# Kernel tuning notes

Measured on AMD Instinct MI355X. Metric: run time of the kernel, lower is better.

The kernel has to match this reference:

```python
import jax, jax.numpy as jnp
import numpy as np

EPS = 1e-7  # utils.add_dummy(eps=True) dummy value


def setup_inputs() -> dict:
    key = jax.random.key(0)
    ks = jax.random.split(key, 8)
    n_mentions, emb = 8192, 1024
    batch, n_ants, pw_emb = 1024, 50, 64
    pair_emb = 3 * emb + pw_emb  # 3136
    hidden = 1024
    return {
        "all_mentions": jax.random.normal(ks[0], (n_mentions, emb), jnp.float32),
        "mentions_batch": jax.random.normal(ks[1], (batch, emb), jnp.float32),
        "pw_batch": jax.random.normal(ks[2], (batch, n_ants, pw_emb), jnp.float32),
        "top_rough_scores_batch": jax.random.normal(ks[3], (batch, n_ants), jnp.float32),
        "W1": jax.random.normal(ks[4], (pair_emb, hidden), jnp.float32) * 0.02,
        "b1": jnp.zeros((hidden,), jnp.float32),
        "W_out": jax.random.normal(ks[5], (hidden, 1), jnp.float32) * 0.02,
        "b_out": jnp.zeros((1,), jnp.float32),
        "top_indices_batch": jax.random.randint(ks[6], (batch, n_ants), 0, n_mentions, jnp.int64),
    }


def reference(all_mentions, mentions_batch, pw_batch, top_rough_scores_batch,
              W1, b1, W_out, b_out, top_indices_batch):
    # gather antecedent embeddings: [batch, n_ants, emb]
    b_mentions = all_mentions[top_indices_batch]
    a_mentions = jnp.broadcast_to(mentions_batch[:, None, :], b_mentions.shape)
    # pair matrix: [batch, n_ants, 3*emb + pw_emb]
    pair = jnp.concatenate([a_mentions, b_mentions, a_mentions * b_mentions, pw_batch], axis=2)
    # FFNN: Linear -> LeakyReLU (dropout is identity in eval) -> Linear(->1)
    h = jax.nn.leaky_relu(jnp.einsum("bnf,fh->bnh", pair, W1) + b1, negative_slope=0.01)
    ffnn = (jnp.einsum("bnh,ho->bno", h, W_out) + b_out)[..., 0]  # [batch, n_ants]
    scores = top_rough_scores_batch + ffnn
    dummy = jnp.full((scores.shape[0], 1), EPS, scores.dtype)
    return jnp.concatenate([dummy, scores], axis=1)  # [batch, n_ants + 1]
```

## Files before the change

### kernel.cpp

```cpp
#include <hip/hip_runtime.h>
#include <cstdint>


typedef short short8 __attribute__((ext_vector_type(8)));
typedef float f32x4 __attribute__((ext_vector_type(4)));

#define BT_STRIDE 100352
#define MT_STRIDE 32768
#define PT_STRIDE 34816

static __device__ __forceinline__ unsigned short f2bf(float x) {
  union { float f; unsigned u; } v; v.f = x;
  unsigned r = v.u + 0x7fffu + ((v.u >> 16) & 1u);
  return (unsigned short)(r >> 16);
}
static __device__ __forceinline__ float bf2f(unsigned short u) {
  union { unsigned u; float f; } v; v.u = ((unsigned)u) << 16;
  return v.f;
}

__global__ void k_packW(const float* __restrict__ W1, unsigned short* __restrict__ BtAll) {
  __shared__ float t[64][65];
  int k0 = blockIdx.x * 64, n0 = blockIdx.y * 64;
  int c = threadIdx.x & 63, r4 = threadIdx.x >> 6;
#pragma unroll
  for (int rr = 0; rr < 16; ++rr) {
    int r = rr * 4 + r4;
    t[r][c] = W1[(size_t)(k0 + r) * 1024 + n0 + c];
  }
  __syncthreads();
#pragma unroll
  for (int qq = 0; qq < 2; ++qq) {
    int q = threadIdx.x * 2 + qq;
    int cc = q >> 3, rg = q & 7;
    short8 v;
#pragma unroll
    for (int e = 0; e < 8; ++e) v[e] = (short)f2bf(t[rg * 8 + e][cc]);
    int ct = (n0 + cc) >> 4;
    int kc = (k0 >> 5) + (rg >> 2);
    int ln = (cc & 15) + ((rg & 3) << 4);
    *(short8*)((char*)BtAll + (size_t)ct * BT_STRIDE + kc * 1024 + ln * 16) = v;
  }
}

__global__ void k_cvt(const float* __restrict__ s, unsigned short* __restrict__ d, int n4) {
  int i = blockIdx.x * 256 + threadIdx.x;
  if (i < n4) {
    float4 v = ((const float4*)s)[i];
    ushort4 o; o.x = f2bf(v.x); o.y = f2bf(v.y); o.z = f2bf(v.z); o.w = f2bf(v.w);
    ((ushort4*)d)[i] = o;
  }
}

__global__ void k_packM(const float* __restrict__ am, const float* __restrict__ allm,
                        unsigned short* __restrict__ Mt) {
  int rt = blockIdx.x, t = threadIdx.x;
  const float* S = (rt < 512) ? (allm + (size_t)rt * 16 * 1024)
                              : (am + (size_t)(rt - 512) * 16 * 1024);
  int pf = t & 15, oct = (t >> 4) & 3, kcl = t >> 6;
  const float* row = S + (size_t)pf * 1024;
  char* dst = (char*)Mt + (size_t)rt * MT_STRIDE + (t & 63) * 16;
#pragma unroll
  for (int pass = 0; pass < 8; ++pass) {
    int kc = pass * 4 + kcl;
    int k = kc * 32 + oct * 8;
    float4 v0 = *(const float4*)(row + k);
    float4 v1 = *(const float4*)(row + k + 4);
    short8 o;
    o[0] = (short)f2bf(v0.x); o[1] = (short)f2bf(v0.y);
    o[2] = (short)f2bf(v0.z); o[3] = (short)f2bf(v0.w);
    o[4] = (short)f2bf(v1.x); o[5] = (short)f2bf(v1.y);
    o[6] = (short)f2bf(v1.z); o[7] = (short)f2bf(v1.w);
    *(short8*)(dst + kc * 1024) = o;
  }
}

__global__ void k_pairs(const unsigned short* __restrict__ Abm,
                        const unsigned short* __restrict__ Aball,
                        const float* __restrict__ pw, const int* __restrict__ idx,
                        unsigned short* __restrict__ Pt) {
  __shared__ int g16[16];
  int rt = blockIdx.x, t = threadIdx.x;
  if (t < 16) g16[t] = idx[rt * 16 + t];
  __syncthreads();
  int pf = t & 15, oct = (t >> 4) & 3, kcl = t >> 6;
  int p = rt * 16 + pf;
  const unsigned short* arow = Abm + (size_t)(p / 50) * 1024;
  const unsigned short* brow = Aball + (size_t)g16[pf] * 1024;
  char* dst = (char*)Pt + (size_t)rt * PT_STRIDE + (t & 63) * 16;
#pragma unroll
  for (int pass = 0; pass < 8; ++pass) {
    int kc = pass * 4 + kcl;
    int k = kc * 32 + oct * 8;
    short8 a8 = *(const short8*)(arow + k);
    short8 b8 = *(const short8*)(brow + k);
    short8 o;
#pragma unroll
    for (int e = 0; e < 8; ++e)
      o[e] = (short)f2bf(bf2f((unsigned short)a8[e]) * bf2f((unsigned short)b8[e]));
    *(short8*)(dst + kc * 1024) = o;
  }
  if (t < 128) {
    int kc = 32 + (t >> 6);
    int kpw = (t >> 6) * 32 + oct * 8;
    const float* prow = pw + (size_t)p * 64;
    float4 v0 = *(const float4*)(prow + kpw);
    float4 v1 = *(const float4*)(prow + kpw + 4);
    short8 o;
    o[0] = (short)f2bf(v0.x); o[1] = (short)f2bf(v0.y);
    o[2] = (short)f2bf(v0.z); o[3] = (short)f2bf(v0.w);
    o[4] = (short)f2bf(v1.x); o[5] = (short)f2bf(v1.y);
    o[6] = (short)f2bf(v1.z); o[7] = (short)f2bf(v1.w);
    *(short8*)(dst + kc * 1024) = o;
  }
}

template <int MODE>
__global__ __launch_bounds__(256, 2) void k_gt(
    const unsigned short* __restrict__ At, const unsigned short* __restrict__ BtAll,
    float* __restrict__ C, float* __restrict__ partial,
    const float* __restrict__ Hab, const float* __restrict__ b1,
    const float* __restrict__ Wout, const int* __restrict__ idx) {
  constexpr int NKC = MODE ? 34 : 32;
  constexpr int A_STRIDE = MODE ? PT_STRIDE : MT_STRIDE;
  int tid = threadIdx.x, lane = tid & 63, wave = tid >> 6;
  int llo = lane & 15, lhi = lane >> 4;
  int id = blockIdx.x;
  int x, y;
  if (MODE == 1) {
    int r = id >> 3;
    x = (id & 7) * 100 + (r >> 1);
    y = r & 1;
  } else {
    x = id >> 1;
    y = id & 1;
  }
  int kcoff = MODE ? 64 : ((x < 128) ? 32 : 0);
  int row0 = x * 64;
  int n0w = y * 512 + wave * 128;
  const char* pa = (const char*)At + (size_t)(row0 >> 4) * A_STRIDE + lane * 16;
  const char* pb = (const char*)BtAll + (size_t)(n0w >> 4) * BT_STRIDE +
                   (size_t)kcoff * 1024 + lane * 16;

  f32x4 acc[4][8] = {};
  short8 aA[4], bA[8], aB[4], bB[8];
#pragma unroll
  for (int m = 0; m < 4; ++m) aA[m] = *(const short8*)(pa + (size_t)m * A_STRIDE);
#pragma unroll
  for (int n = 0; n < 8; ++n) bA[n] = *(const short8*)(pb + (size_t)n * BT_STRIDE);
  for (int kt = 0; kt < NKC; kt += 2) {
#pragma unroll
    for (int m = 0; m < 4; ++m)
      aB[m] = *(const short8*)(pa + (size_t)m * A_STRIDE + (kt + 1) * 1024);
#pragma unroll
    for (int n = 0; n < 8; ++n)
      bB[n] = *(const short8*)(pb + (size_t)n * BT_STRIDE + (kt + 1) * 1024);
#pragma unroll
    for (int m = 0; m < 4; ++m)
#pragma unroll
      for (int n = 0; n < 8; ++n)
        acc[m][n] = __builtin_amdgcn_mfma_f32_16x16x32_bf16(aA[m], bA[n], acc[m][n], 0, 0, 0);
    if (kt + 2 < NKC) {
#pragma unroll
      for (int m = 0; m < 4; ++m)
        aA[m] = *(const short8*)(pa + (size_t)m * A_STRIDE + (kt + 2) * 1024);
#pragma unroll
      for (int n = 0; n < 8; ++n)
        bA[n] = *(const short8*)(pb + (size_t)n * BT_STRIDE + (kt + 2) * 1024);
    }
#pragma unroll
    for (int m = 0; m < 4; ++m)
#pragma unroll
      for (int n = 0; n < 8; ++n)
        acc[m][n] = __builtin_amdgcn_mfma_f32_16x16x32_bf16(aB[m], bB[n], acc[m][n], 0, 0, 0);
  }

  if (MODE == 0) {
#pragma unroll
    for (int m = 0; m < 4; ++m)
#pragma unroll
      for (int i = 0; i < 4; ++i) {
        int row = row0 + m * 16 + lhi * 4 + i;
#pragma unroll
        for (int n = 0; n < 8; ++n)
          C[(size_t)row * 1024 + n0w + n * 16 + llo] = acc[m][n][i];
      }
  } else {
    float b1v[8], wov[8];
    int coln[8];
#pragma unroll
    for (int n = 0; n < 8; ++n) {
      coln[n] = n0w + n * 16 + llo;
      b1v[n] = b1[coln[n]];
      wov[n] = Wout[coln[n]];
    }
    int chunk = n0w >> 6;
#pragma unroll
    for (int m = 0; m < 4; ++m)
#pragma unroll
      for (int i = 0; i < 4; ++i) {
        int p = row0 + m * 16 + lhi * 4 + i;
        int bb = p / 50;
        int gg = idx[p];
        const float* Har = Hab + (size_t)(8192 + bb) * 1024;
        const float* Hbr = Hab + (size_t)gg * 1024;
        float s0 = 0.f, s1 = 0.f;
#pragma unroll
        for (int n = 0; n < 4; ++n) {
          float h = acc[m][n][i] + Har[coln[n]] + Hbr[coln[n]] + b1v[n];
          h = h > 0.f ? h : 0.01f * h;
          s0 += h * wov[n];
        }
#pragma unroll
        for (int n = 4; n < 8; ++n) {
          float h = acc[m][n][i] + Har[coln[n]] + Hbr[coln[n]] + b1v[n];
          h = h > 0.f ? h : 0.01f * h;
          s1 += h * wov[n];
        }
        s0 += __shfl_xor(s0, 1, 64);
        s0 += __shfl_xor(s0, 2, 64);
        s0 += __shfl_xor(s0, 4, 64);
        s0 += __shfl_xor(s0, 8, 64);
        s1 += __shfl_xor(s1, 1, 64);
        s1 += __shfl_xor(s1, 2, 64);
        s1 += __shfl_xor(s1, 4, 64);
        s1 += __shfl_xor(s1, 8, 64);
        if (llo == 0) {
          partial[(size_t)p * 16 + chunk + 0] = s0;
          partial[(size_t)p * 16 + chunk + 1] = s1;
        }
      }
  }
}

__global__ void k_final(const float* __restrict__ partial, const float* __restrict__ rough,
                        const float* __restrict__ bout, float* __restrict__ out) {
  int t = blockIdx.x * 256 + threadIdx.x;
  if (t < 51200) {
    float s = rough[t] + bout[0];
    const float* pp = partial + (size_t)t * 16;
#pragma unroll
    for (int c = 0; c < 16; ++c) s += pp[c];
    out[(size_t)(t / 50) * 51 + 1 + (t % 50)] = s;
  }
  if (t < 1024) out[(size_t)t * 51] = 1e-7f;
}

extern "C" void kernel_launch(void* const* d_in, const int* in_sizes, int n_in,
                              void* d_out, int out_size, void* d_ws, size_t ws_size,
                              hipStream_t stream) {
  (void)in_sizes; (void)n_in; (void)out_size;
  const float* allm  = (const float*)d_in[0];
  const float* am    = (const float*)d_in[1];
  const float* pw    = (const float*)d_in[2];
  const float* rough = (const float*)d_in[3];
  const float* W1    = (const float*)d_in[4];
  const float* b1    = (const float*)d_in[5];
  const float* Wout  = (const float*)d_in[6];
  const float* bout  = (const float*)d_in[7];
  const int*   idx   = (const int*)d_in[8];
  float* out = (float*)d_out;

  char* w = (char*)d_ws;
  unsigned short* BtAll = (unsigned short*)w; w += (size_t)64 * BT_STRIDE;
  unsigned short* Mt    = (unsigned short*)w; w += (size_t)576 * MT_STRIDE;
  unsigned short* Abm   = (unsigned short*)w; w += (size_t)1024 * 1024 * 2;
  unsigned short* Aball = (unsigned short*)w; w += (size_t)8192 * 1024 * 2;
  unsigned short* Pt    = (unsigned short*)w; w += (size_t)3200 * PT_STRIDE;
  float* Hab            = (float*)w;          w += (size_t)9216 * 1024 * 4;
  float* part           = (float*)w;          w += (size_t)51200 * 16 * 4;
  size_t need = (size_t)(w - (char*)d_ws);
  if (ws_size < need) return;

  k_packW<<<dim3(49, 16), 256, 0, stream>>>(W1, BtAll);
  k_cvt<<<dim3(1024), 256, 0, stream>>>(am, Abm, 1024 * 1024 / 4);
  k_cvt<<<dim3(8192), 256, 0, stream>>>(allm, Aball, 8192 * 1024 / 4);
  k_packM<<<dim3(576), 256, 0, stream>>>(am, allm, Mt);
  k_pairs<<<dim3(3200), 256, 0, stream>>>(Abm, Aball, pw, idx, Pt);
  k_gt<0><<<dim3(288), 256, 0, stream>>>(Mt, BtAll, Hab, nullptr,
                                         nullptr, nullptr, nullptr, nullptr);
  k_gt<1><<<dim3(1600), 256, 0, stream>>>(Pt, BtAll, nullptr, part,
                                          Hab, b1, Wout, idx);
  k_final<<<dim3(200), 256, 0, stream>>>(part, rough, bout, out);
}
```

Before: 254.1 us.

## Enlarge GEMM wave tiles to 128x128 with interleaved fragment layout

```diff
diff --git a/kernel.cpp b/kernel.cpp
--- a/kernel.cpp
+++ b/kernel.cpp
@@ -5,9 +5,9 @@
 typedef short short8 __attribute__((ext_vector_type(8)));
 typedef float f32x4 __attribute__((ext_vector_type(4)));
 
-#define BT_STRIDE 100352
-#define MT_STRIDE 32768
-#define PT_STRIDE 34816
+#define PT2_RT 278528ULL
+#define MT2_RT 262144ULL
+#define BT2_CT 802816ULL
 
 static __device__ __forceinline__ unsigned short f2bf(float x) {
   union { float f; unsigned u; } v; v.f = x;
@@ -19,7 +19,7 @@
   return v.f;
 }
 
-__global__ void k_packW(const float* __restrict__ W1, unsigned short* __restrict__ BtAll) {
+__global__ void k_packW(const float* __restrict__ W1, unsigned short* __restrict__ Bt2) {
   __shared__ float t[64][65];
   int k0 = blockIdx.x * 64, n0 = blockIdx.y * 64;
   int c = threadIdx.x & 63, r4 = threadIdx.x >> 6;
@@ -36,10 +36,11 @@
     short8 v;
 #pragma unroll
     for (int e = 0; e < 8; ++e) v[e] = (short)f2bf(t[rg * 8 + e][cc]);
-    int ct = (n0 + cc) >> 4;
+    int col = n0 + cc;
+    int ct = col >> 7, nf = (col >> 4) & 7;
     int kc = (k0 >> 5) + (rg >> 2);
-    int ln = (cc & 15) + ((rg & 3) << 4);
-    *(short8*)((char*)BtAll + (size_t)ct * BT_STRIDE + kc * 1024 + ln * 16) = v;
+    int ln = (col & 15) + ((rg & 3) << 4);
+    *(short8*)((char*)Bt2 + (size_t)ct * BT2_CT + (size_t)kc * 8192 + nf * 1024 + ln * 16) = v;
   }
 }
 
@@ -53,13 +54,14 @@
 }
 
 __global__ void k_packM(const float* __restrict__ am, const float* __restrict__ allm,
-                        unsigned short* __restrict__ Mt) {
-  int rt = blockIdx.x, t = threadIdx.x;
-  const float* S = (rt < 512) ? (allm + (size_t)rt * 16 * 1024)
-                              : (am + (size_t)(rt - 512) * 16 * 1024);
+                        unsigned short* __restrict__ Mt2) {
+  int bid = blockIdx.x, t = threadIdx.x;
+  int rt = bid >> 3, mf = bid & 7;
   int pf = t & 15, oct = (t >> 4) & 3, kcl = t >> 6;
-  const float* row = S + (size_t)pf * 1024;
-  char* dst = (char*)Mt + (size_t)rt * MT_STRIDE + (t & 63) * 16;
+  int grow = bid * 16 + pf;
+  const float* row = (grow < 8192) ? (allm + (size_t)grow * 1024)
+                                   : (am + (size_t)(grow - 8192) * 1024);
+  char* dst = (char*)Mt2 + (size_t)rt * MT2_RT + mf * 1024 + (t & 63) * 16;
 #pragma unroll
   for (int pass = 0; pass < 8; ++pass) {
     int kc = pass * 4 + kcl;
@@ -71,23 +73,25 @@
     o[2] = (short)f2bf(v0.z); o[3] = (short)f2bf(v0.w);
     o[4] = (short)f2bf(v1.x); o[5] = (short)f2bf(v1.y);
     o[6] = (short)f2bf(v1.z); o[7] = (short)f2bf(v1.w);
-    *(short8*)(dst + kc * 1024) = o;
+    *(short8*)(dst + (size_t)kc * 8192) = o;
   }
 }
 
 __global__ void k_pairs(const unsigned short* __restrict__ Abm,
                         const unsigned short* __restrict__ Aball,
                         const float* __restrict__ pw, const int* __restrict__ idx,
-                        unsigned short* __restrict__ Pt) {
+                        unsigned short* __restrict__ Pt2) {
   __shared__ int g16[16];
-  int rt = blockIdx.x, t = threadIdx.x;
-  if (t < 16) g16[t] = idx[rt * 16 + t];
+  int bid = blockIdx.x, t = threadIdx.x;
+  int rt = bid >> 3, mf = bid & 7;
+  int p0 = bid * 16;
+  if (t < 16) g16[t] = idx[p0 + t];
   __syncthreads();
   int pf = t & 15, oct = (t >> 4) & 3, kcl = t >> 6;
-  int p = rt * 16 + pf;
+  int p = p0 + pf;
   const unsigned short* arow = Abm + (size_t)(p / 50) * 1024;
   const unsigned short* brow = Aball + (size_t)g16[pf] * 1024;
-  char* dst = (char*)Pt + (size_t)rt * PT_STRIDE + (t & 63) * 16;
+  char* dst = (char*)Pt2 + (size_t)rt * PT2_RT + mf * 1024 + (t & 63) * 16;
 #pragma unroll
   for (int pass = 0; pass < 8; ++pass) {
     int kc = pass * 4 + kcl;
@@ -98,7 +102,7 @@
 #pragma unroll
     for (int e = 0; e < 8; ++e)
       o[e] = (short)f2bf(bf2f((unsigned short)a8[e]) * bf2f((unsigned short)b8[e]));
-    *(short8*)(dst + kc * 1024) = o;
+    *(short8*)(dst + (size_t)kc * 8192) = o;
   }
   if (t < 128) {
     int kc = 32 + (t >> 6);
@@ -111,65 +115,69 @@
     o[2] = (short)f2bf(v0.z); o[3] = (short)f2bf(v0.w);
     o[4] = (short)f2bf(v1.x); o[5] = (short)f2bf(v1.y);
     o[6] = (short)f2bf(v1.z); o[7] = (short)f2bf(v1.w);
-    *(short8*)(dst + kc * 1024) = o;
+    *(short8*)(dst + (size_t)kc * 8192) = o;
   }
 }
 
 template <int MODE>
-__global__ __launch_bounds__(256, 2) void k_gt(
-    const unsigned short* __restrict__ At, const unsigned short* __restrict__ BtAll,
+__global__ __launch_bounds__(256, 1) void k_gt(
+    const unsigned short* __restrict__ At, const unsigned short* __restrict__ Bt2,
     float* __restrict__ C, float* __restrict__ partial,
     const float* __restrict__ Hab, const float* __restrict__ b1,
     const float* __restrict__ Wout, const int* __restrict__ idx) {
   constexpr int NKC = MODE ? 34 : 32;
-  constexpr int A_STRIDE = MODE ? PT_STRIDE : MT_STRIDE;
+  constexpr size_t ART = MODE ? PT2_RT : MT2_RT;
   int tid = threadIdx.x, lane = tid & 63, wave = tid >> 6;
+  int wr = wave >> 1, wc = wave & 1;
   int llo = lane & 15, lhi = lane >> 4;
   int id = blockIdx.x;
   int x, y;
   if (MODE == 1) {
     int r = id >> 3;
-    x = (id & 7) * 100 + (r >> 1);
-    y = r & 1;
+    x = (id & 7) * 25 + (r >> 2);
+    y = r & 3;
   } else {
-    x = id >> 1;
-    y = id & 1;
-  }
-  int kcoff = MODE ? 64 : ((x < 128) ? 32 : 0);
-  int row0 = x * 64;
-  int n0w = y * 512 + wave * 128;
-  const char* pa = (const char*)At + (size_t)(row0 >> 4) * A_STRIDE + lane * 16;
-  const char* pb = (const char*)BtAll + (size_t)(n0w >> 4) * BT_STRIDE +
-                   (size_t)kcoff * 1024 + lane * 16;
-
-  f32x4 acc[4][8] = {};
-  short8 aA[4], bA[8], aB[4], bB[8];
-#pragma unroll
-  for (int m = 0; m < 4; ++m) aA[m] = *(const short8*)(pa + (size_t)m * A_STRIDE);
-#pragma unroll
-  for (int n = 0; n < 8; ++n) bA[n] = *(const short8*)(pb + (size_t)n * BT_STRIDE);
+    x = id >> 2;
+    y = id & 3;
+  }
+  int kcoff = MODE ? 64 : ((x < 32) ? 32 : 0);
+  int rt = x * 2 + wr;
+  int ct = y * 2 + wc;
+  int row0 = rt * 128;
+  int n0w = ct * 128;
+  const char* pa = (const char*)At + (size_t)rt * ART + lane * 16;
+  const char* pb = (const char*)Bt2 + (size_t)ct * BT2_CT + (size_t)kcoff * 8192 + lane * 16;
+
+  f32x4 acc[8][8] = {};
+  short8 aA[8], bA[8], aB[8], bB[8];
+#pragma unroll
+  for (int m = 0; m < 8; ++m) aA[m] = *(const short8*)(pa + m * 1024);
+#pragma unroll
+  for (int n = 0; n < 8; ++n) bA[n] = *(const short8*)(pb + n * 1024);
   for (int kt = 0; kt < NKC; kt += 2) {
-#pragma unroll
-    for (int m = 0; m < 4; ++m)
-      aB[m] = *(const short8*)(pa + (size_t)m * A_STRIDE + (kt + 1) * 1024);
-#pragma unroll
-    for (int n = 0; n < 8; ++n)
-      bB[n] = *(const short8*)(pb + (size_t)n * BT_STRIDE + (kt + 1) * 1024);
-#pragma unroll
-    for (int m = 0; m < 4; ++m)
+    {
+      const char* pa1 = pa + (size_t)(kt + 1) * 8192;
+      const char* pb1 = pb + (size_t)(kt + 1) * 8192;
+#pragma unroll
+      for (int m = 0; m < 8; ++m) aB[m] = *(const short8*)(pa1 + m * 1024);
+#pragma unroll
+      for (int n = 0; n < 8; ++n) bB[n] = *(const short8*)(pb1 + n * 1024);
+    }
+#pragma unroll
+    for (int m = 0; m < 8; ++m)
 #pragma unroll
       for (int n = 0; n < 8; ++n)
         acc[m][n] = __builtin_amdgcn_mfma_f32_16x16x32_bf16(aA[m], bA[n], acc[m][n], 0, 0, 0);
     if (kt + 2 < NKC) {
-#pragma unroll
-      for (int m = 0; m < 4; ++m)
-        aA[m] = *(const short8*)(pa + (size_t)m * A_STRIDE + (kt + 2) * 1024);
-#pragma unroll
-      for (int n = 0; n < 8; ++n)
-        bA[n] = *(const short8*)(pb + (size_t)n * BT_STRIDE + (kt + 2) * 1024);
+      const char* pa2 = pa + (size_t)(kt + 2) * 8192;
+      const char* pb2 = pb + (size_t)(kt + 2) * 8192;
+#pragma unroll
+      for (int m = 0; m < 8; ++m) aA[m] = *(const short8*)(pa2 + m * 1024);
+#pragma unroll
+      for (int n = 0; n < 8; ++n) bA[n] = *(const short8*)(pb2 + n * 1024);
     }
 #pragma unroll
-    for (int m = 0; m < 4; ++m)
+    for (int m = 0; m < 8; ++m)
 #pragma unroll
       for (int n = 0; n < 8; ++n)
         acc[m][n] = __builtin_amdgcn_mfma_f32_16x16x32_bf16(aB[m], bB[n], acc[m][n], 0, 0, 0);
@@ -177,7 +185,7 @@
 
   if (MODE == 0) {
 #pragma unroll
-    for (int m = 0; m < 4; ++m)
+    for (int m = 0; m < 8; ++m)
 #pragma unroll
       for (int i = 0; i < 4; ++i) {
         int row = row0 + m * 16 + lhi * 4 + i;
@@ -196,7 +204,7 @@
     }
     int chunk = n0w >> 6;
 #pragma unroll
-    for (int m = 0; m < 4; ++m)
+    for (int m = 0; m < 8; ++m)
 #pragma unroll
       for (int i = 0; i < 4; ++i) {
         int p = row0 + m * 16 + lhi * 4 + i;
@@ -262,24 +270,24 @@
   float* out = (float*)d_out;
 
   char* w = (char*)d_ws;
-  unsigned short* BtAll = (unsigned short*)w; w += (size_t)64 * BT_STRIDE;
-  unsigned short* Mt    = (unsigned short*)w; w += (size_t)576 * MT_STRIDE;
+  unsigned short* Bt2   = (unsigned short*)w; w += (size_t)8 * BT2_CT;
+  unsigned short* Mt2   = (unsigned short*)w; w += (size_t)72 * MT2_RT;
   unsigned short* Abm   = (unsigned short*)w; w += (size_t)1024 * 1024 * 2;
   unsigned short* Aball = (unsigned short*)w; w += (size_t)8192 * 1024 * 2;
-  unsigned short* Pt    = (unsigned short*)w; w += (size_t)3200 * PT_STRIDE;
+  unsigned short* Pt2   = (unsigned short*)w; w += (size_t)400 * PT2_RT;
   float* Hab            = (float*)w;          w += (size_t)9216 * 1024 * 4;
   float* part           = (float*)w;          w += (size_t)51200 * 16 * 4;
   size_t need = (size_t)(w - (char*)d_ws);
   if (ws_size < need) return;
 
-  k_packW<<<dim3(49, 16), 256, 0, stream>>>(W1, BtAll);
+  k_packW<<<dim3(49, 16), 256, 0, stream>>>(W1, Bt2);
   k_cvt<<<dim3(1024), 256, 0, stream>>>(am, Abm, 1024 * 1024 / 4);
   k_cvt<<<dim3(8192), 256, 0, stream>>>(allm, Aball, 8192 * 1024 / 4);
-  k_packM<<<dim3(576), 256, 0, stream>>>(am, allm, Mt);
-  k_pairs<<<dim3(3200), 256, 0, stream>>>(Abm, Aball, pw, idx, Pt);
-  k_gt<0><<<dim3(288), 256, 0, stream>>>(Mt, BtAll, Hab, nullptr,
+  k_packM<<<dim3(576), 256, 0, stream>>>(am, allm, Mt2);
+  k_pairs<<<dim3(3200), 256, 0, stream>>>(Abm, Aball, pw, idx, Pt2);
+  k_gt<0><<<dim3(144), 256, 0, stream>>>(Mt2, Bt2, Hab, nullptr,
                                          nullptr, nullptr, nullptr, nullptr);
-  k_gt<1><<<dim3(1600), 256, 0, stream>>>(Pt, BtAll, nullptr, part,
-                                          Hab, b1, Wout, idx);
+  k_gt<1><<<dim3(800), 256, 0, stream>>>(Pt2, Bt2, nullptr, part,
+                                         Hab, b1, Wout, idx);
   k_final<<<dim3(200), 256, 0, stream>>>(part, rough, bout, out);
 }
```

Result: slower. 338.0 us (+33.0%).
